# Optimization experiments

Measured on AMD Instinct MI355X. Metric: run time of the kernel, lower is better.

## Reference

```python
import jax, jax.numpy as jnp
import numpy as np

N = 100000      # nodes
E = 1600000     # edges (avg degree 16)
DIN, DH, DOUT = 128, 64, 32


def setup_inputs() -> dict:
    key = jax.random.key(0)
    ks = jax.random.split(key, 6)
    x = jax.random.normal(ks[0], (N, DIN), dtype=jnp.float32)
    edge_index = jax.random.randint(ks[1], (2, E), 0, N, dtype=jnp.int32)
    # GCNConv weights (glorot-ish scale), biases zero-init as in PyG default
    W1 = jax.random.normal(ks[2], (DIN, DH), dtype=jnp.float32) / np.sqrt(DIN).astype(np.float32)
    b1 = jnp.zeros((DH,), dtype=jnp.float32)
    W2 = jax.random.normal(ks[3], (DH, DOUT), dtype=jnp.float32) / np.sqrt(DH).astype(np.float32)
    b2 = jnp.zeros((DOUT,), dtype=jnp.float32)
    # fc is hard-reset in reset_parameters: weight=ones, bias=zeros
    fc_w = jnp.ones((1, DOUT), dtype=jnp.float32)
    fc_b = jnp.zeros((1,), dtype=jnp.float32)
    return {"x": x, "edge_index": edge_index, "W1": W1, "b1": b1,
            "W2": W2, "b2": b2, "fc_w": fc_w, "fc_b": fc_b}


def gcn_conv(x, W, b, src, dst, n):
    """PyG GCNConv: add self-loops, symmetric deg normalization, x@W then aggregate."""
    h = x @ W                                             # [n, dout] transform first
    ones = jnp.ones(src.shape[0], dtype=x.dtype)
    deg = jax.ops.segment_sum(ones, dst, num_segments=n) + 1.0   # +1 for self-loop
    dinv = jax.lax.rsqrt(deg)
    coef = dinv[src] * dinv[dst]                          # [E] edge norm
    agg = jax.ops.segment_sum(h[src] * coef[:, None], dst, num_segments=n)
    agg = agg + h * (1.0 / deg)[:, None]                  # self-loop term: dinv_i*dinv_i
    return agg + b


def reference(x, edge_index, W1, b1, W2, b2, fc_w, fc_b):
    src, dst = edge_index[0], edge_index[1]
    h = jax.nn.relu(gcn_conv(x, W1, b1, src, dst, N))
    h = jax.nn.relu(gcn_conv(h, W2, b2, src, dst, N))
    scores = (h @ fc_w.T + fc_b)[:, 0]                    # Linear(out,1) then squeeze
    return scores, h
```

## Files before the change

### kernel.cpp

```cpp
#include <hip/hip_runtime.h>

#define NN 100000
#define EE 1600000
#define DIN 128
#define DH 64
#define DOUT 32

#define BSH 8
#define BNODES 256
#define NBUCK ((NN + BNODES - 1) / BNODES)
#define BCAP 4608
#define CHUNK 4096
#define NCHUNK ((EE + CHUNK - 1) / CHUNK)

typedef unsigned short ush;
typedef __attribute__((ext_vector_type(8))) short bf16x8;
typedef __attribute__((ext_vector_type(4))) float f32x4;
typedef __attribute__((ext_vector_type(2))) float f32x2;

__device__ __forceinline__ float bflo(unsigned u) {
    union { unsigned u; float f; } c; c.u = u << 16; return c.f;
}
__device__ __forceinline__ float bfhi(unsigned u) {
    union { unsigned u; float f; } c; c.u = u & 0xffff0000u; return c.f;
}
__device__ __forceinline__ ush f2bf(float f) {
    union { float f; unsigned u; } c; c.f = f;
    unsigned r = c.u + 0x7fff + ((c.u >> 16) & 1);
    return (ush)(r >> 16);
}

__device__ __forceinline__ void pka(f32x2& a, f32x2 b) {
    asm("v_pk_add_f32 %0, %0, %1" : "+v"(a) : "v"(b));
}
__device__ __forceinline__ void pkfma(f32x2& d, f32x2 a, f32x2 b) {
    asm("v_pk_fma_f32 %0, %1, %2, %0" : "+v"(d) : "v"(a), "v"(b));
}
__device__ __forceinline__ void pkmul(f32x2& a, f32x2 b) {
    asm("v_pk_mul_f32 %0, %0, %1" : "+v"(a) : "v"(b));
}
__device__ __forceinline__ f32x2 up2(unsigned u) {
    f32x2 p; p.x = bflo(u); p.y = bfhi(u); return p;
}

__global__ void init_bcur_kernel(int* __restrict__ bcur) {
    int i = blockIdx.x * 256 + threadIdx.x;
    if (i < NBUCK) bcur[i] = i * BCAP;
}

__global__ __launch_bounds__(256) void binA_kernel(const int* __restrict__ src,
                                                   const int* __restrict__ dst,
                                                   int* __restrict__ bcur,
                                                   unsigned* __restrict__ tmp) {
    __shared__ int hist[NBUCK];
    __shared__ int scn[NBUCK];
    __shared__ int cur[NBUCK];
    __shared__ int gb[NBUCK];
    __shared__ int s2[256];
    __shared__ unsigned staged[CHUNK];
    __shared__ int gaddr[CHUNK];
    int t = threadIdx.x;
    for (int i = t; i < NBUCK; i += 256) hist[i] = 0;
    __syncthreads();
    int e0 = blockIdx.x * CHUNK;
    int nE = min(CHUNK, EE - e0);

    int my_e[16], my_bk[16];
#pragma unroll
    for (int k = 0; k < 16; k++) {
        int li = t + k * 256;
        bool ok = li < nE;
        int idx = ok ? (e0 + li) : e0;
        int d = dst[idx];
        int s = src[idx];
        int b = d >> BSH;
        my_e[k] = (s << 8) | (d & 255);
        my_bk[k] = ok ? b : -1;
        if (ok) atomicAdd(&hist[b], 1);
    }
    __syncthreads();
    int a0 = (2 * t < NBUCK) ? hist[2 * t] : 0;
    int a1 = (2 * t + 1 < NBUCK) ? hist[2 * t + 1] : 0;
    s2[t] = a0 + a1;
    __syncthreads();
    for (int off = 1; off < 256; off <<= 1) {
        int x = (t >= off) ? s2[t - off] : 0;
        __syncthreads();
        s2[t] += x;
        __syncthreads();
    }
    int excl = s2[t] - a0 - a1;
    if (2 * t < NBUCK)     { scn[2 * t] = excl;          cur[2 * t] = excl; }
    if (2 * t + 1 < NBUCK) { scn[2 * t + 1] = excl + a0; cur[2 * t + 1] = excl + a0; }
    __syncthreads();
    for (int i = t; i < NBUCK; i += 256) {
        int h = hist[i];
        if (h) gb[i] = atomicAdd(&bcur[i], h) - scn[i];
    }
    __syncthreads();
#pragma unroll
    for (int k = 0; k < 16; k++) {
        int b = my_bk[k];
        if (b >= 0) {
            int lp = atomicAdd(&cur[b], 1);
            staged[lp] = (unsigned)my_e[k];
            gaddr[lp] = gb[b] + lp;
        }
    }
    __syncthreads();
    for (int i = t; i < nE; i += 256)
        tmp[gaddr[i]] = staged[i];
}

__global__ __launch_bounds__(256) void binB_kernel(const unsigned* __restrict__ tmp,
                                                   const int* __restrict__ bcur,
                                                   int* __restrict__ csr,
                                                   int* __restrict__ offs,
                                                   int* __restrict__ ends,
                                                   float* __restrict__ dinv) {
    __shared__ int hist[BNODES], cur[BNODES], sc[BNODES];
    int b = blockIdx.x, t = threadIdx.x;
    int e0 = b * BCAP, e1 = bcur[b];
    hist[t] = 0;
    __syncthreads();
    for (int i = e0 + t; i < e1; i += 256) atomicAdd(&hist[tmp[i] & 255], 1);
    __syncthreads();
    int v = hist[t];
    sc[t] = v;
    __syncthreads();
    for (int off = 1; off < 256; off <<= 1) {
        int x = (t >= off) ? sc[t - off] : 0;
        __syncthreads();
        sc[t] += x;
        __syncthreads();
    }
    int excl = sc[t] - v;
    cur[t] = e0 + excl;
    int node = (b << BSH) + t;
    if (node < NN) {
        offs[node] = e0 + excl;
        ends[node] = e0 + excl + v;
        dinv[node] = 1.0f / sqrtf((float)v + 1.0f);
    }
    __syncthreads();
    for (int i = e0 + t; i < e1; i += 256) {
        unsigned u = tmp[i];
        int pos = atomicAdd(&cur[u & 255], 1);
        csr[pos] = (int)(u >> 8);
    }
}

template <int K, int NC, typename XT>
__global__ __launch_bounds__(256) void gemm_mfma_kernel(const XT* __restrict__ X,
                                                        const float* __restrict__ W,
                                                        const float* __restrict__ dinv,
                                                        ush* __restrict__ Y) {
    constexpr int GROWS = 128;
    constexpr int KP = K + 8;
    constexpr int NKC = K / 32;
    constexpr int NCT = NC / 16;
    __shared__ __align__(16) ush Xl[GROWS * KP];
    __shared__ __align__(16) ush Wt[NC * KP];
    const int t = threadIdx.x;
    const int row0 = blockIdx.x * GROWS;

    if constexpr (sizeof(XT) == 4) {
        for (int i = t; i < GROWS * (K / 4); i += 256) {
            int r = i / (K / 4), c4 = i % (K / 4);
            int row = row0 + r;
            float4 v = make_float4(0.f, 0.f, 0.f, 0.f);
            if (row < NN) v = *(const float4*)&X[(size_t)row * K + c4 * 4];
            ushort4 o;
            o.x = f2bf(v.x); o.y = f2bf(v.y); o.z = f2bf(v.z); o.w = f2bf(v.w);
            *(ushort4*)&Xl[r * KP + c4 * 4] = o;
        }
    } else {
        for (int i = t; i < GROWS * (K / 8); i += 256) {
            int r = i / (K / 8), c8 = i % (K / 8);
            int row = row0 + r;
            uint4 v = make_uint4(0, 0, 0, 0);
            if (row < NN) v = *(const uint4*)&X[(size_t)row * K + c8 * 8];
            *(uint4*)&Xl[r * KP + c8 * 8] = v;
        }
    }
    for (int i = t; i < K * (NC / 4); i += 256) {
        int k = i / (NC / 4), n4 = i % (NC / 4);
        float4 v = *(const float4*)&W[k * NC + n4 * 4];
        Wt[(n4 * 4 + 0) * KP + k] = f2bf(v.x);
        Wt[(n4 * 4 + 1) * KP + k] = f2bf(v.y);
        Wt[(n4 * 4 + 2) * KP + k] = f2bf(v.z);
        Wt[(n4 * 4 + 3) * KP + k] = f2bf(v.w);
    }
    __syncthreads();

    const int wave = t >> 6, lane = t & 63;
    const int m = lane & 15, quad = lane >> 4;
    const int wrow = wave * 32;

    f32x4 acc[2][NCT];
#pragma unroll
    for (int rt = 0; rt < 2; rt++)
#pragma unroll
        for (int ct = 0; ct < NCT; ct++) acc[rt][ct] = (f32x4){0.f, 0.f, 0.f, 0.f};

#pragma unroll
    for (int kc = 0; kc < NKC; kc++) {
        int koff = kc * 32 + quad * 8;
        bf16x8 b[NCT];
#pragma unroll
        for (int ct = 0; ct < NCT; ct++)
            b[ct] = *(const bf16x8*)&Wt[(ct * 16 + m) * KP + koff];
#pragma unroll
        for (int rt = 0; rt < 2; rt++) {
            bf16x8 a = *(const bf16x8*)&Xl[(wrow + rt * 16 + m) * KP + koff];
#pragma unroll
            for (int ct = 0; ct < NCT; ct++)
                acc[rt][ct] = __builtin_amdgcn_mfma_f32_16x16x32_bf16(a, b[ct], acc[rt][ct], 0, 0, 0);
        }
    }
#pragma unroll
    for (int rt = 0; rt < 2; rt++) {
#pragma unroll
        for (int reg = 0; reg < 4; reg++) {
            int row = row0 + wrow + rt * 16 + quad * 4 + reg;
            if (row < NN) {
                float s = dinv[row];
#pragma unroll
                for (int ct = 0; ct < NCT; ct++)
                    Y[(size_t)row * NC + ct * 16 + m] = f2bf(acc[rt][ct][reg] * s);
            }
        }
    }
}

#define ACCP(u4) { pka(ac0, up2(u4.x)); pka(ac1, up2(u4.y)); \
                   pka(ac2, up2(u4.z)); pka(ac3, up2(u4.w)); }

#define ZINV(u4, v) { u4.x = (v) ? u4.x : 0u; u4.y = (v) ? u4.y : 0u; \
                      u4.z = (v) ? u4.z : 0u; u4.w = (v) ? u4.w : 0u; }

#define BFLY(msk) { f32x2 t_;                                           \
    t_.x = __shfl_xor(ac0.x, msk); t_.y = __shfl_xor(ac0.y, msk); pka(ac0, t_); \
    t_.x = __shfl_xor(ac1.x, msk); t_.y = __shfl_xor(ac1.y, msk); pka(ac1, t_); \
    t_.x = __shfl_xor(ac2.x, msk); t_.y = __shfl_xor(ac2.y, msk); pka(ac2, t_); \
    t_.x = __shfl_xor(ac3.x, msk); t_.y = __shfl_xor(ac3.y, msk); pka(ac3, t_); }

__global__ __launch_bounds__(256) void gather1_fused_kernel(const int* __restrict__ offs,
                                                            const int* __restrict__ ends,
                                                            const float* __restrict__ dinv,
                                                            const ush* __restrict__ Hs,
                                                            const int* __restrict__ csr,
                                                            const float* __restrict__ b1,
                                                            const float* __restrict__ W2,
                                                            ush* __restrict__ Hs2) {
    __shared__ __align__(16) float Wp[32 * 68];
    {
        int t = threadIdx.x;
        int lp = t >> 3, r = t & 7;
        int srow = (lp & 7) * 8 + r, scol = (lp >> 3) * 8;
        float4 va = *(const float4*)&W2[srow * DOUT + scol];
        float4 vb = *(const float4*)&W2[srow * DOUT + scol + 4];
        *(float4*)&Wp[lp * 68 + r * 8] = va;
        *(float4*)&Wp[lp * 68 + r * 8 + 4] = vb;
    }
    __syncthreads();

    int wid = (blockIdx.x * 256 + threadIdx.x) >> 6;
    int lane = threadIdx.x & 63;
    int node = wid * 2 + (lane >> 5);
    if (node >= NN) return;
    int l = lane & 31;
    int es = l >> 3;
    int fg = l & 7;
    int start = offs[node], end = ends[node];
    float dv = dinv[node];
    uint4 su = *(const uint4*)&Hs[node * DH + fg * 8];
    f32x2 ac0 = {0.f, 0.f}, ac1 = {0.f, 0.f}, ac2 = {0.f, 0.f}, ac3 = {0.f, 0.f};

    int base = start + es;
    {
        int p0 = base, p1 = base + 4, p2 = base + 8,
            p3 = base + 12, p4 = base + 16, p5 = base + 20;
        bool v0 = p0 < end, v1 = p1 < end, v2 = p2 < end,
             v3 = p3 < end, v4 = p4 < end, v5 = p5 < end;
        int s0 = csr[v0 ? p0 : 0], s1 = csr[v1 ? p1 : 0], s2 = csr[v2 ? p2 : 0],
            s3 = csr[v3 ? p3 : 0], s4 = csr[v4 ? p4 : 0], s5 = csr[v5 ? p5 : 0];
        uint4 u0 = *(const uint4*)&Hs[s0 * DH + fg * 8];
        uint4 u1 = *(const uint4*)&Hs[s1 * DH + fg * 8];
        uint4 u2 = *(const uint4*)&Hs[s2 * DH + fg * 8];
        uint4 u3 = *(const uint4*)&Hs[s3 * DH + fg * 8];
        uint4 u4 = *(const uint4*)&Hs[s4 * DH + fg * 8];
        uint4 u5 = *(const uint4*)&Hs[s5 * DH + fg * 8];
        ZINV(u0, v0) ZINV(u1, v1) ZINV(u2, v2)
        ZINV(u3, v3) ZINV(u4, v4) ZINV(u5, v5)
        ACCP(u0) ACCP(u1) ACCP(u2) ACCP(u3) ACCP(u4) ACCP(u5)
    }
    for (int k = base + 24; k < end; k += 4) {
        int s = csr[k];
        uint4 u = *(const uint4*)&Hs[s * DH + fg * 8];
        ACCP(u)
    }
    BFLY(8) BFLY(16)

    float4 ba = *(const float4*)&b1[fg * 8];
    float4 bb = *(const float4*)&b1[fg * 8 + 4];
    f32x2 dvp; dvp.x = dv; dvp.y = dv;
    pka(ac0, up2(su.x)); pka(ac1, up2(su.y)); pka(ac2, up2(su.z)); pka(ac3, up2(su.w));
    f32x2 h0; h0.x = ba.x; h0.y = ba.y;
    f32x2 h1; h1.x = ba.z; h1.y = ba.w;
    f32x2 h2; h2.x = bb.x; h2.y = bb.y;
    f32x2 h3; h3.x = bb.z; h3.y = bb.w;
    pkfma(h0, dvp, ac0); pkfma(h1, dvp, ac1); pkfma(h2, dvp, ac2); pkfma(h3, dvp, ac3);
    h0.x = fmaxf(h0.x, 0.f); h0.y = fmaxf(h0.y, 0.f);
    h1.x = fmaxf(h1.x, 0.f); h1.y = fmaxf(h1.y, 0.f);
    h2.x = fmaxf(h2.x, 0.f); h2.y = fmaxf(h2.y, 0.f);
    h3.x = fmaxf(h3.x, 0.f); h3.y = fmaxf(h3.y, 0.f);

    const float* wl = &Wp[l * 68];
    float hs_[8] = {h0.x, h0.y, h1.x, h1.y, h2.x, h2.y, h3.x, h3.y};
    f32x2 p0 = {0.f, 0.f}, p1 = {0.f, 0.f}, p2 = {0.f, 0.f}, p3 = {0.f, 0.f};
#pragma unroll
    for (int r = 0; r < 8; r++) {
        float4 wa = *(const float4*)&wl[r * 8];
        float4 wb = *(const float4*)&wl[r * 8 + 4];
        f32x2 hr; hr.x = hs_[r]; hr.y = hs_[r];
        f32x2 w01; w01.x = wa.x; w01.y = wa.y;
        f32x2 w23; w23.x = wa.z; w23.y = wa.w;
        f32x2 w45; w45.x = wb.x; w45.y = wb.y;
        f32x2 w67; w67.x = wb.z; w67.y = wb.w;
        pkfma(p0, hr, w01); pkfma(p1, hr, w23);
        pkfma(p2, hr, w45); pkfma(p3, hr, w67);
    }
#pragma unroll
    for (int msk = 1; msk <= 4; msk <<= 1) {
        f32x2 t_;
        t_.x = __shfl_xor(p0.x, msk); t_.y = __shfl_xor(p0.y, msk); pka(p0, t_);
        t_.x = __shfl_xor(p1.x, msk); t_.y = __shfl_xor(p1.y, msk); pka(p1, t_);
        t_.x = __shfl_xor(p2.x, msk); t_.y = __shfl_xor(p2.y, msk); pka(p2, t_);
        t_.x = __shfl_xor(p3.x, msk); t_.y = __shfl_xor(p3.y, msk); pka(p3, t_);
    }
    if (fg == 0) {
        pkmul(p0, dvp); pkmul(p1, dvp); pkmul(p2, dvp); pkmul(p3, dvp);
        ushort4 oa, ob;
        oa.x = f2bf(p0.x); oa.y = f2bf(p0.y); oa.z = f2bf(p1.x); oa.w = f2bf(p1.y);
        ob.x = f2bf(p2.x); ob.y = f2bf(p2.y); ob.z = f2bf(p3.x); ob.w = f2bf(p3.y);
        *(ushort4*)&Hs2[node * DOUT + es * 8] = oa;
        *(ushort4*)&Hs2[node * DOUT + es * 8 + 4] = ob;
    }
}

__global__ __launch_bounds__(256) void gather2_kernel(const int* __restrict__ offs,
                                                      const int* __restrict__ ends,
                                                      const float* __restrict__ dinv,
                                                      const ush* __restrict__ Hs,
                                                      const int* __restrict__ csr,
                                                      const float* __restrict__ b2,
                                                      const float* __restrict__ fcw,
                                                      const float* __restrict__ fcb,
                                                      float* __restrict__ h2,
                                                      float* __restrict__ scores) {
    int wid = (blockIdx.x * 256 + threadIdx.x) >> 6;
    int lane = threadIdx.x & 63;
    int node = wid * 2 + (lane >> 5);
    if (node >= NN) return;
    int l = lane & 31;
    int es = l >> 2;
    int fg = l & 3;
    int start = offs[node], end = ends[node];
    float dv = dinv[node];
    uint4 su = *(const uint4*)&Hs[node * DOUT + fg * 8];
    f32x2 ac0 = {0.f, 0.f}, ac1 = {0.f, 0.f}, ac2 = {0.f, 0.f}, ac3 = {0.f, 0.f};

    int base = start + es;
    {
        int p0 = base, p1 = base + 8, p2 = base + 16, p3 = base + 24;
        bool v0 = p0 < end, v1 = p1 < end, v2 = p2 < end, v3 = p3 < end;
        int s0 = csr[v0 ? p0 : 0], s1 = csr[v1 ? p1 : 0],
            s2 = csr[v2 ? p2 : 0], s3 = csr[v3 ? p3 : 0];
        uint4 u0 = *(const uint4*)&Hs[s0 * DOUT + fg * 8];
        uint4 u1 = *(const uint4*)&Hs[s1 * DOUT + fg * 8];
        uint4 u2 = *(const uint4*)&Hs[s2 * DOUT + fg * 8];
        uint4 u3 = *(const uint4*)&Hs[s3 * DOUT + fg * 8];
        ZINV(u0, v0) ZINV(u1, v1) ZINV(u2, v2) ZINV(u3, v3)
        ACCP(u0) ACCP(u1) ACCP(u2) ACCP(u3)
    }
    for (int k = base + 32; k < end; k += 8) {
        int s = csr[k];
        uint4 u = *(const uint4*)&Hs[s * DOUT + fg * 8];
        ACCP(u)
    }
    BFLY(4) BFLY(8) BFLY(16)

    float4 ba = *(const float4*)&b2[fg * 8];
    float4 bb = *(const float4*)&b2[fg * 8 + 4];
    f32x2 dvp; dvp.x = dv; dvp.y = dv;
    pka(ac0, up2(su.x)); pka(ac1, up2(su.y)); pka(ac2, up2(su.z)); pka(ac3, up2(su.w));
    f32x2 h0; h0.x = ba.x; h0.y = ba.y;
    f32x2 h1; h1.x = ba.z; h1.y = ba.w;
    f32x2 h2v; h2v.x = bb.x; h2v.y = bb.y;
    f32x2 h3; h3.x = bb.z; h3.y = bb.w;
    pkfma(h0, dvp, ac0); pkfma(h1, dvp, ac1); pkfma(h2v, dvp, ac2); pkfma(h3, dvp, ac3);
    h0.x = fmaxf(h0.x, 0.f); h0.y = fmaxf(h0.y, 0.f);
    h1.x = fmaxf(h1.x, 0.f); h1.y = fmaxf(h1.y, 0.f);
    h2v.x = fmaxf(h2v.x, 0.f); h2v.y = fmaxf(h2v.y, 0.f);
    h3.x = fmaxf(h3.x, 0.f); h3.y = fmaxf(h3.y, 0.f);
    if (es == 0) {
        float4 o0, o1;
        o0.x = h0.x; o0.y = h0.y; o0.z = h1.x; o0.w = h1.y;
        o1.x = h2v.x; o1.y = h2v.y; o1.z = h3.x; o1.w = h3.y;
        *(float4*)&h2[node * DOUT + fg * 8] = o0;
        *(float4*)&h2[node * DOUT + fg * 8 + 4] = o1;
    }
    float4 fa = *(const float4*)&fcw[fg * 8];
    float4 fb = *(const float4*)&fcw[fg * 8 + 4];
    f32x2 dp = {0.f, 0.f};
    f32x2 f01; f01.x = fa.x; f01.y = fa.y;
    f32x2 f23; f23.x = fa.z; f23.y = fa.w;
    f32x2 f45; f45.x = fb.x; f45.y = fb.y;
    f32x2 f67; f67.x = fb.z; f67.y = fb.w;
    pkfma(dp, h0, f01); pkfma(dp, h1, f23); pkfma(dp, h2v, f45); pkfma(dp, h3, f67);
    float sv = dp.x + dp.y;
    sv += __shfl_xor(sv, 1); sv += __shfl_xor(sv, 2);
    if (l == 0) scores[node] = sv + fcb[0];
}

extern "C" void kernel_launch(void* const* d_in, const int* in_sizes, int n_in,
                              void* d_out, int out_size, void* d_ws, size_t ws_size,
                              hipStream_t stream) {
    const float* x   = (const float*)d_in[0];
    const int*   ei  = (const int*)d_in[1];
    const float* W1  = (const float*)d_in[2];
    const float* b1  = (const float*)d_in[3];
    const float* W2  = (const float*)d_in[4];
    const float* b2  = (const float*)d_in[5];
    const float* fcw = (const float*)d_in[6];
    const float* fcb = (const float*)d_in[7];
    const int* src = ei;
    const int* dst = ei + EE;

    float* ws = (float*)d_ws;
    float* dinv    = ws;
    int*   offs    = (int*)(ws + 100352);
    int*   ends    = (int*)(ws + 200704);
    int*   bcur    = (int*)(ws + 301056);
    int*   csr     = (int*)(ws + 301568);
    unsigned* tmp  = (unsigned*)(ws + 2103296);
    ush*   Hs1     = (ush*)(ws + 3905024);
    ush*   Hs2     = (ush*)(ws + 7105024);

    float* out    = (float*)d_out;
    float* scores = out;
    float* h2     = out + NN;

    const int T = 256;
    init_bcur_kernel<<<2, 256, 0, stream>>>(bcur);
    binA_kernel<<<NCHUNK, T, 0, stream>>>(src, dst, bcur, tmp);
    binB_kernel<<<NBUCK, T, 0, stream>>>(tmp, bcur, csr, offs, ends, dinv);
    gemm_mfma_kernel<DIN, DH, float><<<(NN + 127) / 128, T, 0, stream>>>(x, W1, dinv, Hs1);
    gather1_fused_kernel<<<(NN / 2 * 64 + T - 1) / T, T, 0, stream>>>(offs, ends, dinv, Hs1, csr, b1, W2, Hs2);
    gather2_kernel<<<(NN / 2 * 64 + T - 1) / T, T, 0, stream>>>(offs, ends, dinv, Hs2, csr, b2, fcw, fcb, h2, scores);
}
```

Measured before the change: 214.4 us.

## Merge CSR bucket sort and layer-1 GEMM into one kernel via global degree counts

binA now also counts per-node degrees with global atomics, so the second binning pass no longer needs its histogram and the layer-1 GEMM can compute dinv itself. The CSR build and the GEMM then run as disjoint block ranges of a single launch, removing one kernel launch and the serialization between them. The GEMM also reads x directly from global memory into MFMA fragments instead of staging it through LDS. In exchange there are 1.6M extra global atomics in binA, and the direct x loads may be less coalesced.

```diff
diff --git a/kernel.cpp b/kernel.cpp
--- a/kernel.cpp
+++ b/kernel.cpp
@@ -12,6 +12,7 @@
 #define BCAP 4608
 #define CHUNK 4096
 #define NCHUNK ((EE + CHUNK - 1) / CHUNK)
+#define GEMMB ((NN + 127) / 128)
 
 typedef unsigned short ush;
 typedef __attribute__((ext_vector_type(8))) short bf16x8;
@@ -43,14 +44,16 @@
     f32x2 p; p.x = bflo(u); p.y = bfhi(u); return p;
 }
 
-__global__ void init_bcur_kernel(int* __restrict__ bcur) {
+__global__ void init_kernel(int* __restrict__ gdeg, int* __restrict__ bcur) {
     int i = blockIdx.x * 256 + threadIdx.x;
+    if (i < NN) gdeg[i] = 0;
     if (i < NBUCK) bcur[i] = i * BCAP;
 }
 
 __global__ __launch_bounds__(256) void binA_kernel(const int* __restrict__ src,
                                                    const int* __restrict__ dst,
                                                    int* __restrict__ bcur,
+                                                   int* __restrict__ gdeg,
                                                    unsigned* __restrict__ tmp) {
     __shared__ int hist[NBUCK];
     __shared__ int scn[NBUCK];
@@ -76,7 +79,10 @@
         int b = d >> BSH;
         my_e[k] = (s << 8) | (d & 255);
         my_bk[k] = ok ? b : -1;
-        if (ok) atomicAdd(&hist[b], 1);
+        if (ok) {
+            atomicAdd(&hist[b], 1);
+            atomicAdd(&gdeg[d], 1);
+        }
     }
     __syncthreads();
     int a0 = (2 * t < NBUCK) ? hist[2 * t] : 0;
@@ -112,80 +118,55 @@
         tmp[gaddr[i]] = staged[i];
 }
 
-__global__ __launch_bounds__(256) void binB_kernel(const unsigned* __restrict__ tmp,
-                                                   const int* __restrict__ bcur,
-                                                   int* __restrict__ csr,
-                                                   int* __restrict__ offs,
-                                                   int* __restrict__ ends,
-                                                   float* __restrict__ dinv) {
-    __shared__ int hist[BNODES], cur[BNODES], sc[BNODES];
-    int b = blockIdx.x, t = threadIdx.x;
-    int e0 = b * BCAP, e1 = bcur[b];
-    hist[t] = 0;
-    __syncthreads();
-    for (int i = e0 + t; i < e1; i += 256) atomicAdd(&hist[tmp[i] & 255], 1);
-    __syncthreads();
-    int v = hist[t];
-    sc[t] = v;
-    __syncthreads();
-    for (int off = 1; off < 256; off <<= 1) {
-        int x = (t >= off) ? sc[t - off] : 0;
+__global__ __launch_bounds__(256) void fatBG_kernel(const unsigned* __restrict__ tmp,
+                                                    const int* __restrict__ bcur,
+                                                    const int* __restrict__ gdeg,
+                                                    const float* __restrict__ x,
+                                                    const float* __restrict__ W1,
+                                                    int* __restrict__ csr,
+                                                    int* __restrict__ offs,
+                                                    int* __restrict__ ends,
+                                                    float* __restrict__ dinv,
+                                                    ush* __restrict__ Hs1) {
+    __shared__ int cur[BNODES], sc[BNODES];
+    constexpr int KP = DIN + 8;
+    __shared__ __align__(16) ush Wt[DH * KP];
+    const int t = threadIdx.x;
+
+    if (blockIdx.x < NBUCK) {
+        int b = blockIdx.x;
+        int e0 = b * BCAP, e1 = bcur[b];
+        int node = (b << BSH) + t;
+        int v = (node < NN) ? gdeg[node] : 0;
+        sc[t] = v;
         __syncthreads();
-        sc[t] += x;
+        for (int off = 1; off < 256; off <<= 1) {
+            int xv = (t >= off) ? sc[t - off] : 0;
+            __syncthreads();
+            sc[t] += xv;
+            __syncthreads();
+        }
+        int excl = sc[t] - v;
+        cur[t] = e0 + excl;
+        if (node < NN) {
+            offs[node] = e0 + excl;
+            ends[node] = e0 + excl + v;
+            dinv[node] = 1.0f / sqrtf((float)v + 1.0f);
+        }
         __syncthreads();
-    }
-    int excl = sc[t] - v;
-    cur[t] = e0 + excl;
-    int node = (b << BSH) + t;
-    if (node < NN) {
-        offs[node] = e0 + excl;
-        ends[node] = e0 + excl + v;
-        dinv[node] = 1.0f / sqrtf((float)v + 1.0f);
-    }
-    __syncthreads();
-    for (int i = e0 + t; i < e1; i += 256) {
-        unsigned u = tmp[i];
-        int pos = atomicAdd(&cur[u & 255], 1);
-        csr[pos] = (int)(u >> 8);
-    }
-}
-
-template <int K, int NC, typename XT>
-__global__ __launch_bounds__(256) void gemm_mfma_kernel(const XT* __restrict__ X,
-                                                        const float* __restrict__ W,
-                                                        const float* __restrict__ dinv,
-                                                        ush* __restrict__ Y) {
-    constexpr int GROWS = 128;
-    constexpr int KP = K + 8;
-    constexpr int NKC = K / 32;
-    constexpr int NCT = NC / 16;
-    __shared__ __align__(16) ush Xl[GROWS * KP];
-    __shared__ __align__(16) ush Wt[NC * KP];
-    const int t = threadIdx.x;
-    const int row0 = blockIdx.x * GROWS;
-
-    if constexpr (sizeof(XT) == 4) {
-        for (int i = t; i < GROWS * (K / 4); i += 256) {
-            int r = i / (K / 4), c4 = i % (K / 4);
-            int row = row0 + r;
-            float4 v = make_float4(0.f, 0.f, 0.f, 0.f);
-            if (row < NN) v = *(const float4*)&X[(size_t)row * K + c4 * 4];
-            ushort4 o;
-            o.x = f2bf(v.x); o.y = f2bf(v.y); o.z = f2bf(v.z); o.w = f2bf(v.w);
-            *(ushort4*)&Xl[r * KP + c4 * 4] = o;
-        }
-    } else {
-        for (int i = t; i < GROWS * (K / 8); i += 256) {
-            int r = i / (K / 8), c8 = i % (K / 8);
-            int row = row0 + r;
-            uint4 v = make_uint4(0, 0, 0, 0);
-            if (row < NN) v = *(const uint4*)&X[(size_t)row * K + c8 * 8];
-            *(uint4*)&Xl[r * KP + c8 * 8] = v;
-        }
-    }
-    for (int i = t; i < K * (NC / 4); i += 256) {
-        int k = i / (NC / 4), n4 = i % (NC / 4);
-        float4 v = *(const float4*)&W[k * NC + n4 * 4];
+        for (int i = e0 + t; i < e1; i += 256) {
+            unsigned u = tmp[i];
+            int pos = atomicAdd(&cur[u & 255], 1);
+            csr[pos] = (int)(u >> 8);
+        }
+        return;
+    }
+
+    const int row0 = (blockIdx.x - NBUCK) * 128;
+    constexpr int NCT = DH / 16;
+    for (int i = t; i < DIN * (DH / 4); i += 256) {
+        int k = i / (DH / 4), n4 = i % (DH / 4);
+        float4 v = *(const float4*)&W1[k * DH + n4 * 4];
         Wt[(n4 * 4 + 0) * KP + k] = f2bf(v.x);
         Wt[(n4 * 4 + 1) * KP + k] = f2bf(v.y);
         Wt[(n4 * 4 + 2) * KP + k] = f2bf(v.z);
@@ -204,18 +185,26 @@
         for (int ct = 0; ct < NCT; ct++) acc[rt][ct] = (f32x4){0.f, 0.f, 0.f, 0.f};
 
 #pragma unroll
-    for (int kc = 0; kc < NKC; kc++) {
+    for (int kc = 0; kc < DIN / 32; kc++) {
         int koff = kc * 32 + quad * 8;
-        bf16x8 b[NCT];
+        bf16x8 bfr[NCT];
 #pragma unroll
         for (int ct = 0; ct < NCT; ct++)
-            b[ct] = *(const bf16x8*)&Wt[(ct * 16 + m) * KP + koff];
+            bfr[ct] = *(const bf16x8*)&Wt[(ct * 16 + m) * KP + koff];
 #pragma unroll
         for (int rt = 0; rt < 2; rt++) {
-            bf16x8 a = *(const bf16x8*)&Xl[(wrow + rt * 16 + m) * KP + koff];
+            int row = row0 + wrow + rt * 16 + m;
+            float4 va = make_float4(0.f, 0.f, 0.f, 0.f), vb = va;
+            if (row < NN) {
+                va = *(const float4*)&x[(size_t)row * DIN + koff];
+                vb = *(const float4*)&x[(size_t)row * DIN + koff + 4];
+            }
+            union { bf16x8 v; ush s[8]; } A;
+            A.s[0] = f2bf(va.x); A.s[1] = f2bf(va.y); A.s[2] = f2bf(va.z); A.s[3] = f2bf(va.w);
+            A.s[4] = f2bf(vb.x); A.s[5] = f2bf(vb.y); A.s[6] = f2bf(vb.z); A.s[7] = f2bf(vb.w);
 #pragma unroll
             for (int ct = 0; ct < NCT; ct++)
-                acc[rt][ct] = __builtin_amdgcn_mfma_f32_16x16x32_bf16(a, b[ct], acc[rt][ct], 0, 0, 0);
+                acc[rt][ct] = __builtin_amdgcn_mfma_f32_16x16x32_bf16(A.v, bfr[ct], acc[rt][ct], 0, 0, 0);
         }
     }
 #pragma unroll
@@ -224,10 +213,10 @@
         for (int reg = 0; reg < 4; reg++) {
             int row = row0 + wrow + rt * 16 + quad * 4 + reg;
             if (row < NN) {
-                float s = dinv[row];
+                float s = 1.0f / sqrtf((float)gdeg[row] + 1.0f);
 #pragma unroll
                 for (int ct = 0; ct < NCT; ct++)
-                    Y[(size_t)row * NC + ct * 16 + m] = f2bf(acc[rt][ct][reg] * s);
+                    Hs1[(size_t)row * DH + ct * 16 + m] = f2bf(acc[rt][ct][reg] * s);
             }
         }
     }
@@ -447,16 +436,17 @@
     unsigned* tmp  = (unsigned*)(ws + 2103296);
     ush*   Hs1     = (ush*)(ws + 3905024);
     ush*   Hs2     = (ush*)(ws + 7105024);
+    int*   gdeg    = (int*)(ws + 8705024);
 
     float* out    = (float*)d_out;
     float* scores = out;
     float* h2     = out + NN;
 
     const int T = 256;
-    init_bcur_kernel<<<2, 256, 0, stream>>>(bcur);
-    binA_kernel<<<NCHUNK, T, 0, stream>>>(src, dst, bcur, tmp);
-    binB_kernel<<<NBUCK, T, 0, stream>>>(tmp, bcur, csr, offs, ends, dinv);
-    gemm_mfma_kernel<DIN, DH, float><<<(NN + 127) / 128, T, 0, stream>>>(x, W1, dinv, Hs1);
+    init_kernel<<<(NN + 255) / 256, T, 0, stream>>>(gdeg, bcur);
+    binA_kernel<<<NCHUNK, T, 0, stream>>>(src, dst, bcur, gdeg, tmp);
+    fatBG_kernel<<<NBUCK + GEMMB, T, 0, stream>>>(tmp, bcur, gdeg, x, W1,
+                                                  csr, offs, ends, dinv, Hs1);
     gather1_fused_kernel<<<(NN / 2 * 64 + T - 1) / T, T, 0, stream>>>(offs, ends, dinv, Hs1, csr, b1, W2, Hs2);
     gather2_kernel<<<(NN / 2 * 64 + T - 1) / T, T, 0, stream>>>(offs, ends, dinv, Hs2, csr, b2, fcw, fcb, h2, scores);
 }
```

After: 264.4 us. 1.23x slower.
